# Kernel tuning notes

Measured on AMD Instinct MI355X. Metric: run time of the kernel, lower is better.

The kernel has to match this reference:

```python
import jax, jax.numpy as jnp
import numpy as np

ACT_BIT = 8
W_BIT = 8
EPS = 1e-8


def ste_round(x):
    # straight-through round (matches torch STE quant autograd)
    return x + jax.lax.stop_gradient(jnp.round(x) - x)


def quant_act(x):
    """Per-tensor symmetric 8-bit activation quantization (HAWQ QuantAct)."""
    n = 2 ** (ACT_BIT - 1) - 1  # 127
    x_max = jax.lax.stop_gradient(jnp.max(jnp.abs(x)))
    scale = jnp.maximum(x_max, EPS) / n
    x_int = jnp.clip(ste_round(x / scale), -n - 1, n)
    return x_int * scale, scale


def quant_linear(x_q, act_scale, weight, bias):
    """Per-channel symmetric 8-bit weight quant + integer matmul + fused dequant."""
    n = 2 ** (W_BIT - 1) - 1  # 127
    w_max = jax.lax.stop_gradient(jnp.max(jnp.abs(weight), axis=1, keepdims=True))  # [out,1]
    w_scale = jnp.maximum(w_max, EPS) / n                                            # [out,1]
    w_int = jnp.clip(ste_round(weight / w_scale), -n - 1, n)                         # [out,in]
    bias_scale = w_scale[:, 0] * act_scale                                           # [out]
    b_int = ste_round(bias / bias_scale)                                             # [out]
    x_int = x_q / act_scale                                   # integer-valued float, [..., in]
    out_int = jnp.einsum('...i,oi->...o', x_int, w_int)       # int8-domain GEMM in float
    return (out_int + b_int) * bias_scale                     # fused dequant


def setup_inputs() -> dict:
    key = jax.random.key(0)
    k1, k2, k3 = jax.random.split(key, 3)
    L, B, Q, D, O = 6, 8, 1024, 1024, 1024
    hs = jax.random.normal(k1, (L, B, Q, D), dtype=jnp.float32)
    weight = jax.random.normal(k2, (O, D), dtype=jnp.float32) * 0.02
    bias = jax.random.normal(k3, (O,), dtype=jnp.float32) * 0.02
    return {"hs": hs, "weight": weight, "bias": bias}


def reference(hs, weight, bias):
    x_q, act_scale = quant_act(hs)
    return quant_linear(x_q, act_scale, weight, bias)
```

## Files before the change

### kernel.cpp

```cpp
#include <hip/hip_runtime.h>
#include <stdint.h>

typedef int i32x4 __attribute__((ext_vector_type(4)));

#define K_DIM 1024
#define BM 128
#define BN 128
#define BKK 64
#define NKT (K_DIM / BKK)


__device__ __forceinline__ int quant1(float v, float inv) {
  float t = rintf(v * inv);
  t = fminf(fmaxf(t, -128.0f), 127.0f);
  return (int)t;
}

__device__ __forceinline__ void gld_lds16(const signed char* g, signed char* l) {
  typedef const __attribute__((address_space(1))) unsigned int* gp_t;
  typedef __attribute__((address_space(3))) unsigned int* lp_t;
  __builtin_amdgcn_global_load_lds((gp_t)(const void*)g, (lp_t)(void*)l, 16, 0, 0);
}

#define SB __builtin_amdgcn_sched_barrier(0)
#define BAR __builtin_amdgcn_s_barrier()
#define WAIT_LGKM0 asm volatile("s_waitcnt lgkmcnt(0)" ::: "memory")

__global__ void absmax_part(const float* __restrict__ x, float* __restrict__ parts,
                            long long n4) {
  long long i = (long long)blockIdx.x * blockDim.x + threadIdx.x;
  const long long stride = (long long)gridDim.x * blockDim.x;
  const float4* x4 = (const float4*)x;
  float m = 0.0f;
  for (; i < n4; i += stride) {
    float4 v = x4[i];
    m = fmaxf(m, fmaxf(fmaxf(fabsf(v.x), fabsf(v.y)), fmaxf(fabsf(v.z), fabsf(v.w))));
  }
#pragma unroll
  for (int off = 32; off > 0; off >>= 1) m = fmaxf(m, __shfl_down(m, off, 64));
  __shared__ float sm[4];
  const int lane = threadIdx.x & 63, wid = threadIdx.x >> 6;
  if (lane == 0) sm[wid] = m;
  __syncthreads();
  if (threadIdx.x == 0)
    parts[blockIdx.x] = fmaxf(fmaxf(sm[0], sm[1]), fmaxf(sm[2], sm[3]));
}

__global__ void absmax_fin(const float* __restrict__ parts, unsigned int* __restrict__ amax_u,
                           int nparts) {
  const int t = threadIdx.x;
  float m = 0.0f;
  for (int i = t; i < nparts; i += 256) m = fmaxf(m, parts[i]);
#pragma unroll
  for (int off = 32; off > 0; off >>= 1) m = fmaxf(m, __shfl_down(m, off, 64));
  __shared__ float sm[4];
  const int lane = t & 63, wid = t >> 6;
  if (lane == 0) sm[wid] = m;
  __syncthreads();
  if (t == 0)
    amax_u[0] = __float_as_uint(fmaxf(fmaxf(sm[0], sm[1]), fmaxf(sm[2], sm[3])));
}

__global__ void wquant_kernel(const float* __restrict__ w, const float* __restrict__ bias,
                              const unsigned int* __restrict__ amax_u,
                              signed char* __restrict__ wq,
                              float* __restrict__ bscale, float* __restrict__ bint) {
  const int o = blockIdx.x;
  const int t = threadIdx.x;
  float4 v = ((const float4*)(w + (size_t)o * K_DIM))[t];
  float m = fmaxf(fmaxf(fabsf(v.x), fabsf(v.y)), fmaxf(fabsf(v.z), fabsf(v.w)));
#pragma unroll
  for (int off = 32; off > 0; off >>= 1) m = fmaxf(m, __shfl_down(m, off, 64));
  __shared__ float sm[4];
  __shared__ float s_scale;
  const int lane = t & 63, wid = t >> 6;
  if (lane == 0) sm[wid] = m;
  __syncthreads();
  if (t == 0) {
    float wm = fmaxf(fmaxf(sm[0], sm[1]), fmaxf(sm[2], sm[3]));
    float wsc = fmaxf(wm, 1e-8f) / 127.0f;
    float asc = fmaxf(__uint_as_float(*amax_u), 1e-8f) / 127.0f;
    float bsc = wsc * asc;
    bscale[o] = bsc;
    bint[o] = rintf(bias[o] / bsc);
    s_scale = wsc;
  }
  __syncthreads();
  const float inv = 1.0f / s_scale;
  int q0 = quant1(v.x, inv), q1 = quant1(v.y, inv), q2 = quant1(v.z, inv), q3 = quant1(v.w, inv);
  unsigned int p = (unsigned)(q0 & 255) | ((unsigned)(q1 & 255) << 8) |
                   ((unsigned)(q2 & 255) << 16) | ((unsigned)(q3 & 255) << 24);
  const int F = o >> 4, T = t >> 4;
  const int l = (((t >> 2) & 3) << 4) | (o & 15);
  const int j = (t << 2) & 15;
  *(unsigned int*)(wq + (((size_t)F << 14) + (T << 10) + (l << 4) + j)) = p;
}

__global__ __launch_bounds__(256) void aquant_kernel(
    const float* __restrict__ x, const unsigned int* __restrict__ amax_u,
    uint4* __restrict__ q16) {
  __shared__ unsigned int limg[4096];
  const float asc = fmaxf(__uint_as_float(*amax_u), 1e-8f) / 127.0f;
  const float inv = 1.0f / asc;
  const int F = blockIdx.x;
  const int t = threadIdx.x;
  const int r = t >> 4, kq = t & 15;
  const float* rowp = x + (((size_t)F * 16 + r) << 10);
#pragma unroll
  for (int rep = 0; rep < 16; ++rep) {
    const int fi = rep * 16 + kq;
    float4 v = ((const float4*)rowp)[fi];
    int q0 = quant1(v.x, inv), q1 = quant1(v.y, inv), q2 = quant1(v.z, inv), q3 = quant1(v.w, inv);
    unsigned int p = (unsigned)(q0 & 255) | ((unsigned)(q1 & 255) << 8) |
                     ((unsigned)(q2 & 255) << 16) | ((unsigned)(q3 & 255) << 24);
    const int k0 = fi << 2;
    const int T = k0 >> 6;
    const int l = (((k0 >> 4) & 3) << 4) | r;
    const int j = k0 & 15;
    limg[(T << 8) + (l << 2) + (j >> 2)] = p;
  }
  __syncthreads();
  const uint4* src = (const uint4*)limg;
#pragma unroll
  for (int rep2 = 0; rep2 < 4; ++rep2)
    q16[((size_t)F << 10) + rep2 * 256 + t] = src[rep2 * 256 + t];
}

__global__ __launch_bounds__(256, 3) void gemm_kernel(
    const signed char* __restrict__ A, const signed char* __restrict__ W,
    const float* __restrict__ bscale, const float* __restrict__ bint,
    float* __restrict__ out, int M, int N, int K) {
  extern __shared__ __align__(16) signed char smem[];
  signed char* Abase = smem;

  const int nwg = gridDim.x;
  const int orig = blockIdx.x;
  const int wgid = (orig & 7) * (nwg >> 3) + (orig >> 3);
  const int nbn = N / BN;
  const int bm = wgid / nbn;
  const int bn = wgid % nbn;
  const int m0 = bm * BM, n0 = bn * BN;

  const int tid = threadIdx.x;
  const int lane = tid & 63;
  const int wid = tid >> 6;
  const int wr = wid >> 1;
  const int wc = wid & 1;

  const signed char* gaf = A + (((size_t)(m0 >> 4) + wid) << 14) + (lane << 4);
  const size_t fs4 = (size_t)4 << 14;
  const signed char* gbf = W + (((size_t)(n0 >> 4) + wc * 4) << 14) + (lane << 4);

  i32x4 acc[4][4];
#pragma unroll
  for (int i = 0; i < 4; i++)
#pragma unroll
    for (int j = 0; j < 4; j++) acc[i][j] = (i32x4){0, 0, 0, 0};

  i32x4 af[4];
  i32x4 bfA[4], bfB[4];

#define LOADB(L, tt)                                                           \
  do {                                                                         \
    L[0] = *(const i32x4*)(gbf + ((size_t)0 << 14) + ((tt) << 10));            \
    L[1] = *(const i32x4*)(gbf + ((size_t)1 << 14) + ((tt) << 10));            \
    L[2] = *(const i32x4*)(gbf + ((size_t)2 << 14) + ((tt) << 10));            \
    L[3] = *(const i32x4*)(gbf + ((size_t)3 << 14) + ((tt) << 10));            \
  } while (0)

#define ISSUEA(tt)                                                             \
  do {                                                                         \
    gld_lds16(gaf + ((size_t)(tt) << 10),                                      \
              Abase + ((((tt) & 3) * 8 + wid) << 10));                         \
    gld_lds16(gaf + fs4 + ((size_t)(tt) << 10),                                \
              Abase + ((((tt) & 3) * 8 + wid + 4) << 10));                     \
  } while (0)

#define RD_A(t, i_)                                                            \
  af[i_] = *(const i32x4*)(Abase + ((((t) & 3) * 8 + wr * 4 + (i_)) << 10) + (lane << 4))

#define MFMA16U(U)                                                             \
  do {                                                                         \
    __builtin_amdgcn_s_setprio(1);                                             \
    _Pragma("unroll") for (int i_ = 0; i_ < 4; i_++)                           \
      _Pragma("unroll") for (int j_ = 0; j_ < 4; j_++)                         \
        acc[i_][j_] = __builtin_amdgcn_mfma_i32_16x16x64_i8(                   \
            af[i_], U[j_], acc[i_][j_], 0, 0, 0);                              \
    __builtin_amdgcn_s_setprio(0);                                             \
  } while (0)

#define TILE(t, U, L, DOB, DOA, VMW, DOVM)                                     \
  do {                                                                         \
    if (DOB) LOADB(L, (t) + 1);                                                \
    if (DOA) ISSUEA((t) + 3);                                                  \
    SB;                                                                        \
    RD_A(t, 0); RD_A(t, 1); RD_A(t, 2); RD_A(t, 3);                            \
    MFMA16U(U);                                                                \
    if (DOVM) { asm volatile("s_waitcnt " VMW ::: "memory"); }                 \
    SB; BAR; SB;                                                               \
  } while (0)

  ISSUEA(0); ISSUEA(1); ISSUEA(2);
  LOADB(bfA, 0);
  asm volatile("s_waitcnt vmcnt(8)" ::: "memory");
  SB; BAR; SB;

  TILE(0,  bfA, bfB, 1, 1, "vmcnt(8)", 1);
  TILE(1,  bfB, bfA, 1, 1, "vmcnt(8)", 1);
  TILE(2,  bfA, bfB, 1, 1, "vmcnt(8)", 1);
  TILE(3,  bfB, bfA, 1, 1, "vmcnt(8)", 1);
  TILE(4,  bfA, bfB, 1, 1, "vmcnt(8)", 1);
  TILE(5,  bfB, bfA, 1, 1, "vmcnt(8)", 1);
  TILE(6,  bfA, bfB, 1, 1, "vmcnt(8)", 1);
  TILE(7,  bfB, bfA, 1, 1, "vmcnt(8)", 1);
  TILE(8,  bfA, bfB, 1, 1, "vmcnt(8)", 1);
  TILE(9,  bfB, bfA, 1, 1, "vmcnt(8)", 1);
  TILE(10, bfA, bfB, 1, 1, "vmcnt(8)", 1);
  TILE(11, bfB, bfA, 1, 1, "vmcnt(8)", 1);
  TILE(12, bfA, bfB, 1, 1, "vmcnt(8)", 1);
  TILE(13, bfB, bfA, 1, 0, "vmcnt(6)", 1);
  TILE(14, bfA, bfB, 1, 0, "vmcnt(4)", 1);
  TILE(15, bfB, bfA, 0, 0, "", 0);

#undef TILE
#undef MFMA16U
#undef RD_A
#undef ISSUEA
#undef LOADB

  float* Cst = (float*)smem;
  const int rr = (lane >> 4) * 4;
  const int cc = lane & 15;
#pragma unroll
  for (int h = 0; h < 2; ++h) {
    if (wr == h) {
#pragma unroll
      for (int j = 0; j < 4; j++) {
        const int colL = wc * 64 + j * 16 + cc;
        const float bs = bscale[n0 + colL];
        const float bi = bint[n0 + colL];
#pragma unroll
        for (int i = 0; i < 4; i++)
#pragma unroll
          for (int r = 0; r < 4; r++)
            Cst[(i * 16 + rr + r) * 128 + colL] = ((float)acc[i][j][r] + bi) * bs;
      }
    }
    WAIT_LGKM0;
    BAR;
    const size_t rowbase = (size_t)(m0 + h * 64) * N + n0;
#pragma unroll
    for (int it = 0; it < 8; ++it) {
      const int r_ = it * 8 + wid * 2 + (lane >> 5);
      const int c_ = (lane & 31) * 4;
      float4 v = *(const float4*)&Cst[r_ * 128 + c_];
      *(float4*)&out[rowbase + (size_t)r_ * N + c_] = v;
    }
    WAIT_LGKM0;
    BAR;
  }
}

extern "C" void kernel_launch(void* const* d_in, const int* in_sizes, int n_in,
                              void* d_out, int out_size, void* d_ws, size_t ws_size,
                              hipStream_t stream) {
  const float* hs = (const float*)d_in[0];
  const float* w = (const float*)d_in[1];
  const float* bias = (const float*)d_in[2];
  float* out = (float*)d_out;

  const long long n = (long long)in_sizes[0];
  const int K = K_DIM;
  const int O = in_sizes[2];
  const int M = (int)(n / K);

  char* ws = (char*)d_ws;
  unsigned int* amax_u = (unsigned int*)ws;
  float* parts = (float*)(ws + 1024);
  float* bscale = (float*)(ws + 16384);
  float* bint = (float*)(ws + 20480);
  signed char* wq = (signed char*)(ws + 65536);
  signed char* xq = (signed char*)(ws + 65536 + 1048576);

  const long long n4 = n / 4;
  absmax_part<<<2048, 256, 0, stream>>>(hs, parts, n4);
  absmax_fin<<<1, 256, 0, stream>>>(parts, amax_u, 2048);
  wquant_kernel<<<O, 256, 0, stream>>>(w, bias, amax_u, wq, bscale, bint);
  aquant_kernel<<<M / 16, 256, 0, stream>>>(hs, amax_u, (uint4*)xq);

  const int nblocks = (M / BM) * (O / BN);
  gemm_kernel<<<nblocks, 256, 32768, stream>>>(xq, wq, bscale, bint, out, M, O, K);
}
```

Before: 189.2 us.

## Load A fragments directly from global into registers, dropping LDS staging and barriers

The GEMM main loop no longer stages A tiles in LDS through global_load_lds with a multi-stage ring and per-tile barriers. Each wave now loads its own A and B MFMA fragments straight from global memory into double-buffered registers and alternates load and MFMA sets with no barriers. LDS is kept only as a static buffer for the epilogue transpose. The cost is that each A fragment is fetched by the two waves sharing a row from L2/global instead of once per workgroup, and load latency is hidden only by single-step register prefetch.

```diff
diff --git a/kernel.cpp b/kernel.cpp
--- a/kernel.cpp
+++ b/kernel.cpp
@@ -14,12 +14,6 @@
   float t = rintf(v * inv);
   t = fminf(fmaxf(t, -128.0f), 127.0f);
   return (int)t;
-}
-
-__device__ __forceinline__ void gld_lds16(const signed char* g, signed char* l) {
-  typedef const __attribute__((address_space(1))) unsigned int* gp_t;
-  typedef __attribute__((address_space(3))) unsigned int* lp_t;
-  __builtin_amdgcn_global_load_lds((gp_t)(const void*)g, (lp_t)(void*)l, 16, 0, 0);
 }
 
 #define SB __builtin_amdgcn_sched_barrier(0)
@@ -130,8 +124,7 @@
     const signed char* __restrict__ A, const signed char* __restrict__ W,
     const float* __restrict__ bscale, const float* __restrict__ bint,
     float* __restrict__ out, int M, int N, int K) {
-  extern __shared__ __align__(16) signed char smem[];
-  signed char* Abase = smem;
+  __shared__ __align__(16) float Cst[64 * 128];
 
   const int nwg = gridDim.x;
   const int orig = blockIdx.x;
@@ -147,9 +140,8 @@
   const int wr = wid >> 1;
   const int wc = wid & 1;
 
-  const signed char* gaf = A + (((size_t)(m0 >> 4) + wid) << 14) + (lane << 4);
-  const size_t fs4 = (size_t)4 << 14;
-  const signed char* gbf = W + (((size_t)(n0 >> 4) + wc * 4) << 14) + (lane << 4);
+  const signed char* gA = A + (((size_t)(m0 >> 4) + wr * 4) << 14) + (lane << 4);
+  const signed char* gB = W + (((size_t)(n0 >> 4) + wc * 4) << 14) + (lane << 4);
 
   i32x4 acc[4][4];
 #pragma unroll
@@ -157,82 +149,56 @@
 #pragma unroll
     for (int j = 0; j < 4; j++) acc[i][j] = (i32x4){0, 0, 0, 0};
 
-  i32x4 af[4];
-  i32x4 bfA[4], bfB[4];
-
-#define LOADB(L, tt)                                                           \
+  i32x4 aA[4], aB[4], bA[4], bB[4];
+
+#define LDSET(AR, BR, tt)                                                      \
   do {                                                                         \
-    L[0] = *(const i32x4*)(gbf + ((size_t)0 << 14) + ((tt) << 10));            \
-    L[1] = *(const i32x4*)(gbf + ((size_t)1 << 14) + ((tt) << 10));            \
-    L[2] = *(const i32x4*)(gbf + ((size_t)2 << 14) + ((tt) << 10));            \
-    L[3] = *(const i32x4*)(gbf + ((size_t)3 << 14) + ((tt) << 10));            \
+    AR[0] = *(const i32x4*)(gA + ((size_t)0 << 14) + ((tt) << 10));            \
+    AR[1] = *(const i32x4*)(gA + ((size_t)1 << 14) + ((tt) << 10));            \
+    AR[2] = *(const i32x4*)(gA + ((size_t)2 << 14) + ((tt) << 10));            \
+    AR[3] = *(const i32x4*)(gA + ((size_t)3 << 14) + ((tt) << 10));            \
+    BR[0] = *(const i32x4*)(gB + ((size_t)0 << 14) + ((tt) << 10));            \
+    BR[1] = *(const i32x4*)(gB + ((size_t)1 << 14) + ((tt) << 10));            \
+    BR[2] = *(const i32x4*)(gB + ((size_t)2 << 14) + ((tt) << 10));            \
+    BR[3] = *(const i32x4*)(gB + ((size_t)3 << 14) + ((tt) << 10));            \
   } while (0)
 
-#define ISSUEA(tt)                                                             \
-  do {                                                                         \
-    gld_lds16(gaf + ((size_t)(tt) << 10),                                      \
-              Abase + ((((tt) & 3) * 8 + wid) << 10));                         \
-    gld_lds16(gaf + fs4 + ((size_t)(tt) << 10),                                \
-              Abase + ((((tt) & 3) * 8 + wid + 4) << 10));                     \
-  } while (0)
-
-#define RD_A(t, i_)                                                            \
-  af[i_] = *(const i32x4*)(Abase + ((((t) & 3) * 8 + wr * 4 + (i_)) << 10) + (lane << 4))
-
-#define MFMA16U(U)                                                             \
+#define MFMA16(AR, BR)                                                         \
   do {                                                                         \
     __builtin_amdgcn_s_setprio(1);                                             \
     _Pragma("unroll") for (int i_ = 0; i_ < 4; i_++)                           \
       _Pragma("unroll") for (int j_ = 0; j_ < 4; j_++)                         \
         acc[i_][j_] = __builtin_amdgcn_mfma_i32_16x16x64_i8(                   \
-            af[i_], U[j_], acc[i_][j_], 0, 0, 0);                              \
+            AR[i_], BR[j_], acc[i_][j_], 0, 0, 0);                             \
     __builtin_amdgcn_s_setprio(0);                                             \
   } while (0)
 
-#define TILE(t, U, L, DOB, DOA, VMW, DOVM)                                     \
-  do {                                                                         \
-    if (DOB) LOADB(L, (t) + 1);                                                \
-    if (DOA) ISSUEA((t) + 3);                                                  \
-    SB;                                                                        \
-    RD_A(t, 0); RD_A(t, 1); RD_A(t, 2); RD_A(t, 3);                            \
-    MFMA16U(U);                                                                \
-    if (DOVM) { asm volatile("s_waitcnt " VMW ::: "memory"); }                 \
-    SB; BAR; SB;                                                               \
-  } while (0)
-
-  ISSUEA(0); ISSUEA(1); ISSUEA(2);
-  LOADB(bfA, 0);
-  asm volatile("s_waitcnt vmcnt(8)" ::: "memory");
-  SB; BAR; SB;
-
-  TILE(0,  bfA, bfB, 1, 1, "vmcnt(8)", 1);
-  TILE(1,  bfB, bfA, 1, 1, "vmcnt(8)", 1);
-  TILE(2,  bfA, bfB, 1, 1, "vmcnt(8)", 1);
-  TILE(3,  bfB, bfA, 1, 1, "vmcnt(8)", 1);
-  TILE(4,  bfA, bfB, 1, 1, "vmcnt(8)", 1);
-  TILE(5,  bfB, bfA, 1, 1, "vmcnt(8)", 1);
-  TILE(6,  bfA, bfB, 1, 1, "vmcnt(8)", 1);
-  TILE(7,  bfB, bfA, 1, 1, "vmcnt(8)", 1);
-  TILE(8,  bfA, bfB, 1, 1, "vmcnt(8)", 1);
-  TILE(9,  bfB, bfA, 1, 1, "vmcnt(8)", 1);
-  TILE(10, bfA, bfB, 1, 1, "vmcnt(8)", 1);
-  TILE(11, bfB, bfA, 1, 1, "vmcnt(8)", 1);
-  TILE(12, bfA, bfB, 1, 1, "vmcnt(8)", 1);
-  TILE(13, bfB, bfA, 1, 0, "vmcnt(6)", 1);
-  TILE(14, bfA, bfB, 1, 0, "vmcnt(4)", 1);
-  TILE(15, bfB, bfA, 0, 0, "", 0);
-
-#undef TILE
-#undef MFMA16U
-#undef RD_A
-#undef ISSUEA
-#undef LOADB
-
-  float* Cst = (float*)smem;
+  LDSET(aA, bA, 0);
+  LDSET(aB, bB, 1);  MFMA16(aA, bA);
+  LDSET(aA, bA, 2);  MFMA16(aB, bB);
+  LDSET(aB, bB, 3);  MFMA16(aA, bA);
+  LDSET(aA, bA, 4);  MFMA16(aB, bB);
+  LDSET(aB, bB, 5);  MFMA16(aA, bA);
+  LDSET(aA, bA, 6);  MFMA16(aB, bB);
+  LDSET(aB, bB, 7);  MFMA16(aA, bA);
+  LDSET(aA, bA, 8);  MFMA16(aB, bB);
+  LDSET(aB, bB, 9);  MFMA16(aA, bA);
+  LDSET(aA, bA, 10); MFMA16(aB, bB);
+  LDSET(aB, bB, 11); MFMA16(aA, bA);
+  LDSET(aA, bA, 12); MFMA16(aB, bB);
+  LDSET(aB, bB, 13); MFMA16(aA, bA);
+  LDSET(aA, bA, 14); MFMA16(aB, bB);
+  LDSET(aB, bB, 15); MFMA16(aA, bA);
+  MFMA16(aB, bB);
+
+#undef MFMA16
+#undef LDSET
+
   const int rr = (lane >> 4) * 4;
   const int cc = lane & 15;
 #pragma unroll
   for (int h = 0; h < 2; ++h) {
+    if (h == 1) BAR;
     if (wr == h) {
 #pragma unroll
       for (int j = 0; j < 4; j++) {
@@ -257,7 +223,6 @@
       *(float4*)&out[rowbase + (size_t)r_ * N + c_] = v;
     }
     WAIT_LGKM0;
-    BAR;
   }
 }
 
@@ -289,5 +254,5 @@
   aquant_kernel<<<M / 16, 256, 0, stream>>>(hs, amax_u, (uint4*)xq);
 
   const int nblocks = (M / BM) * (O / BN);
-  gemm_kernel<<<nblocks, 256, 32768, stream>>>(xq, wq, bscale, bint, out, M, O, K);
-}
+  gemm_kernel<<<nblocks, 256, 0, stream>>>(xq, wq, bscale, bint, out, M, O, K);
+}
```

New measurement: 199.4 us. 1.05x slower.

## Enlarge GEMM tiles to 256x256 with 32x32x32 int8 MFMA and direct stores

Applied to the files above, without the earlier changes.

Doubles the GEMM block tile to 256x256 with 512 threads and switches from 16x16x64 to 32x32x32 int8 MFMA. The quantized weight and activation layouts are regrouped into 32-row fragments to match. The epilogue drops the LDS-staged coalesced store and writes scalars straight to global memory. The aim is more operand reuse per loaded byte and fewer, larger MFMAs, at the cost of fewer blocks for the CUs, higher register pressure and less coalesced output writes.

```diff
diff --git a/kernel.cpp b/kernel.cpp
--- a/kernel.cpp
+++ b/kernel.cpp
@@ -2,10 +2,11 @@
 #include <stdint.h>
 
 typedef int i32x4 __attribute__((ext_vector_type(4)));
+typedef int i32x16 __attribute__((ext_vector_type(16)));
 
 #define K_DIM 1024
-#define BM 128
-#define BN 128
+#define BM 256
+#define BN 256
 #define BKK 64
 #define NKT (K_DIM / BKK)
 
@@ -24,7 +25,6 @@
 
 #define SB __builtin_amdgcn_sched_barrier(0)
 #define BAR __builtin_amdgcn_s_barrier()
-#define WAIT_LGKM0 asm volatile("s_waitcnt lgkmcnt(0)" ::: "memory")
 
 __global__ void absmax_part(const float* __restrict__ x, float* __restrict__ parts,
                             long long n4) {
@@ -90,10 +90,10 @@
   int q0 = quant1(v.x, inv), q1 = quant1(v.y, inv), q2 = quant1(v.z, inv), q3 = quant1(v.w, inv);
   unsigned int p = (unsigned)(q0 & 255) | ((unsigned)(q1 & 255) << 8) |
                    ((unsigned)(q2 & 255) << 16) | ((unsigned)(q3 & 255) << 24);
-  const int F = o >> 4, T = t >> 4;
-  const int l = (((t >> 2) & 3) << 4) | (o & 15);
+  const int F = o >> 5, T = t >> 3;
+  const int l = (o & 31) | (((t >> 2) & 1) << 5);
   const int j = (t << 2) & 15;
-  *(unsigned int*)(wq + (((size_t)F << 14) + (T << 10) + (l << 4) + j)) = p;
+  *(unsigned int*)(wq + (((size_t)(F * 32 + T)) << 10) + (l << 4) + j) = p;
 }
 
 __global__ __launch_bounds__(256) void aquant_kernel(
@@ -102,10 +102,11 @@
   __shared__ unsigned int limg[4096];
   const float asc = fmaxf(__uint_as_float(*amax_u), 1e-8f) / 127.0f;
   const float inv = 1.0f / asc;
-  const int F = blockIdx.x;
+  const int b = blockIdx.x;
+  const int F32 = b >> 1, bh = b & 1;
   const int t = threadIdx.x;
   const int r = t >> 4, kq = t & 15;
-  const float* rowp = x + (((size_t)F * 16 + r) << 10);
+  const float* rowp = x + (((size_t)b * 16 + r) << 10);
 #pragma unroll
   for (int rep = 0; rep < 16; ++rep) {
     const int fi = rep * 16 + kq;
@@ -114,19 +115,22 @@
     unsigned int p = (unsigned)(q0 & 255) | ((unsigned)(q1 & 255) << 8) |
                      ((unsigned)(q2 & 255) << 16) | ((unsigned)(q3 & 255) << 24);
     const int k0 = fi << 2;
-    const int T = k0 >> 6;
-    const int l = (((k0 >> 4) & 3) << 4) | r;
+    const int T32 = k0 >> 5;
+    const int hi = (k0 >> 4) & 1;
     const int j = k0 & 15;
-    limg[(T << 8) + (l << 2) + (j >> 2)] = p;
+    limg[(((T32 << 1) | hi) << 6) + (r << 2) + (j >> 2)] = p;
   }
   __syncthreads();
   const uint4* src = (const uint4*)limg;
 #pragma unroll
-  for (int rep2 = 0; rep2 < 4; ++rep2)
-    q16[((size_t)F << 10) + rep2 * 256 + t] = src[rep2 * 256 + t];
-}
-
-__global__ __launch_bounds__(256, 3) void gemm_kernel(
+  for (int rep2 = 0; rep2 < 4; ++rep2) {
+    const int e = rep2 * 256 + t;
+    const int T32 = e >> 5, hs = (e >> 4) & 1, rr = e & 15;
+    q16[(((size_t)(F32 * 32 + T32)) << 6) + (hs * 32 + bh * 16 + rr)] = src[e];
+  }
+}
+
+__global__ __launch_bounds__(512, 2) void gemm_kernel(
     const signed char* __restrict__ A, const signed char* __restrict__ W,
     const float* __restrict__ bscale, const float* __restrict__ bint,
     float* __restrict__ out, int M, int N, int K) {
@@ -144,48 +148,58 @@
   const int tid = threadIdx.x;
   const int lane = tid & 63;
   const int wid = tid >> 6;
-  const int wr = wid >> 1;
-  const int wc = wid & 1;
-
-  const signed char* gaf = A + (((size_t)(m0 >> 4) + wid) << 14) + (lane << 4);
-  const size_t fs4 = (size_t)4 << 14;
-  const signed char* gbf = W + (((size_t)(n0 >> 4) + wc * 4) << 14) + (lane << 4);
-
-  i32x4 acc[4][4];
+  const int wr = wid >> 2;
+  const int wc = wid & 3;
+
+  const signed char* gaf =
+      A + (((size_t)((m0 >> 5) + (wid >> 1)) * 32 + (wid & 1)) << 10) + (lane << 4);
+  const size_t fs8 = (size_t)128 << 10;
+  const signed char* gbf =
+      W + (((size_t)((n0 >> 5) + wc * 2) * 32) << 10) + (lane << 4);
+
+  i32x16 acc[4][2];
 #pragma unroll
   for (int i = 0; i < 4; i++)
 #pragma unroll
-    for (int j = 0; j < 4; j++) acc[i][j] = (i32x4){0, 0, 0, 0};
-
-  i32x4 af[4];
-  i32x4 bfA[4], bfB[4];
+    for (int j = 0; j < 2; j++)
+#pragma unroll
+      for (int r = 0; r < 16; r++) acc[i][j][r] = 0;
+
+  i32x4 af[4][2];
+  i32x4 bA[2][2], bB[2][2];
 
 #define LOADB(L, tt)                                                           \
   do {                                                                         \
-    L[0] = *(const i32x4*)(gbf + ((size_t)0 << 14) + ((tt) << 10));            \
-    L[1] = *(const i32x4*)(gbf + ((size_t)1 << 14) + ((tt) << 10));            \
-    L[2] = *(const i32x4*)(gbf + ((size_t)2 << 14) + ((tt) << 10));            \
-    L[3] = *(const i32x4*)(gbf + ((size_t)3 << 14) + ((tt) << 10));            \
+    L[0][0] = *(const i32x4*)(gbf + (((size_t)(tt) * 2 + 0) << 10));           \
+    L[0][1] = *(const i32x4*)(gbf + (((size_t)(tt) * 2 + 1) << 10));           \
+    L[1][0] = *(const i32x4*)(gbf + ((size_t)1 << 15) + (((size_t)(tt) * 2 + 0) << 10)); \
+    L[1][1] = *(const i32x4*)(gbf + ((size_t)1 << 15) + (((size_t)(tt) * 2 + 1) << 10)); \
   } while (0)
 
 #define ISSUEA(tt)                                                             \
   do {                                                                         \
-    gld_lds16(gaf + ((size_t)(tt) << 10),                                      \
-              Abase + ((((tt) & 3) * 8 + wid) << 10));                         \
-    gld_lds16(gaf + fs4 + ((size_t)(tt) << 10),                                \
-              Abase + ((((tt) & 3) * 8 + wid + 4) << 10));                     \
-  } while (0)
-
-#define RD_A(t, i_)                                                            \
-  af[i_] = *(const i32x4*)(Abase + ((((t) & 3) * 8 + wr * 4 + (i_)) << 10) + (lane << 4))
-
-#define MFMA16U(U)                                                             \
+    gld_lds16(gaf + ((size_t)(tt) << 11),                                      \
+              Abase + ((((tt) & 3) * 16 + wid) << 10));                        \
+    gld_lds16(gaf + fs8 + ((size_t)(tt) << 11),                                \
+              Abase + ((((tt) & 3) * 16 + wid + 8) << 10));                    \
+  } while (0)
+
+#define RD_A(t)                                                                \
+  do {                                                                         \
+    _Pragma("unroll") for (int m_ = 0; m_ < 4; m_++)                           \
+      _Pragma("unroll") for (int k_ = 0; k_ < 2; k_++)                         \
+        af[m_][k_] = *(const i32x4*)(Abase + ((((t) & 3) * 16 +                \
+                        (wr * 4 + m_) * 2 + k_) << 10) + (lane << 4));         \
+  } while (0)
+
+#define MFMA16(U)                                                              \
   do {                                                                         \
     __builtin_amdgcn_s_setprio(1);                                             \
-    _Pragma("unroll") for (int i_ = 0; i_ < 4; i_++)                           \
-      _Pragma("unroll") for (int j_ = 0; j_ < 4; j_++)                         \
-        acc[i_][j_] = __builtin_amdgcn_mfma_i32_16x16x64_i8(                   \
-            af[i_], U[j_], acc[i_][j_], 0, 0, 0);                              \
+    _Pragma("unroll") for (int m_ = 0; m_ < 4; m_++)                           \
+      _Pragma("unroll") for (int g_ = 0; g_ < 2; g_++)                         \
+        _Pragma("unroll") for (int k_ = 0; k_ < 2; k_++)                       \
+          acc[m_][g_] = __builtin_amdgcn_mfma_i32_32x32x32_i8(                 \
+              af[m_][k_], U[g_][k_], acc[m_][g_], 0, 0, 0);                    \
     __builtin_amdgcn_s_setprio(0);                                             \
   } while (0)
 
@@ -194,70 +208,56 @@
     if (DOB) LOADB(L, (t) + 1);                                                \
     if (DOA) ISSUEA((t) + 3);                                                  \
     SB;                                                                        \
-    RD_A(t, 0); RD_A(t, 1); RD_A(t, 2); RD_A(t, 3);                            \
-    MFMA16U(U);                                                                \
+    RD_A(t);                                                                   \
+    MFMA16(U);                                                                 \
     if (DOVM) { asm volatile("s_waitcnt " VMW ::: "memory"); }                 \
     SB; BAR; SB;                                                               \
   } while (0)
 
   ISSUEA(0); ISSUEA(1); ISSUEA(2);
-  LOADB(bfA, 0);
+  LOADB(bA, 0);
   asm volatile("s_waitcnt vmcnt(8)" ::: "memory");
   SB; BAR; SB;
 
-  TILE(0,  bfA, bfB, 1, 1, "vmcnt(8)", 1);
-  TILE(1,  bfB, bfA, 1, 1, "vmcnt(8)", 1);
-  TILE(2,  bfA, bfB, 1, 1, "vmcnt(8)", 1);
-  TILE(3,  bfB, bfA, 1, 1, "vmcnt(8)", 1);
-  TILE(4,  bfA, bfB, 1, 1, "vmcnt(8)", 1);
-  TILE(5,  bfB, bfA, 1, 1, "vmcnt(8)", 1);
-  TILE(6,  bfA, bfB, 1, 1, "vmcnt(8)", 1);
-  TILE(7,  bfB, bfA, 1, 1, "vmcnt(8)", 1);
-  TILE(8,  bfA, bfB, 1, 1, "vmcnt(8)", 1);
-  TILE(9,  bfB, bfA, 1, 1, "vmcnt(8)", 1);
-  TILE(10, bfA, bfB, 1, 1, "vmcnt(8)", 1);
-  TILE(11, bfB, bfA, 1, 1, "vmcnt(8)", 1);
-  TILE(12, bfA, bfB, 1, 1, "vmcnt(8)", 1);
-  TILE(13, bfB, bfA, 1, 0, "vmcnt(6)", 1);
-  TILE(14, bfA, bfB, 1, 0, "vmcnt(4)", 1);
-  TILE(15, bfB, bfA, 0, 0, "", 0);
+  TILE(0,  bA, bB, 1, 1, "vmcnt(8)", 1);
+  TILE(1,  bB, bA, 1, 1, "vmcnt(8)", 1);
+  TILE(2,  bA, bB, 1, 1, "vmcnt(8)", 1);
+  TILE(3,  bB, bA, 1, 1, "vmcnt(8)", 1);
+  TILE(4,  bA, bB, 1, 1, "vmcnt(8)", 1);
+  TILE(5,  bB, bA, 1, 1, "vmcnt(8)", 1);
+  TILE(6,  bA, bB, 1, 1, "vmcnt(8)", 1);
+  TILE(7,  bB, bA, 1, 1, "vmcnt(8)", 1);
+  TILE(8,  bA, bB, 1, 1, "vmcnt(8)", 1);
+  TILE(9,  bB, bA, 1, 1, "vmcnt(8)", 1);
+  TILE(10, bA, bB, 1, 1, "vmcnt(8)", 1);
+  TILE(11, bB, bA, 1, 1, "vmcnt(8)", 1);
+  TILE(12, bA, bB, 1, 1, "vmcnt(8)", 1);
+  TILE(13, bB, bA, 1, 0, "vmcnt(6)", 1);
+  TILE(14, bA, bB, 1, 0, "vmcnt(4)", 1);
+  TILE(15, bB, bA, 0, 0, "", 0);
 
 #undef TILE
-#undef MFMA16U
+#undef MFMA16
 #undef RD_A
 #undef ISSUEA
 #undef LOADB
 
-  float* Cst = (float*)smem;
-  const int rr = (lane >> 4) * 4;
-  const int cc = lane & 15;
-#pragma unroll
-  for (int h = 0; h < 2; ++h) {
-    if (wr == h) {
-#pragma unroll
-      for (int j = 0; j < 4; j++) {
-        const int colL = wc * 64 + j * 16 + cc;
-        const float bs = bscale[n0 + colL];
-        const float bi = bint[n0 + colL];
-#pragma unroll
-        for (int i = 0; i < 4; i++)
-#pragma unroll
-          for (int r = 0; r < 4; r++)
-            Cst[(i * 16 + rr + r) * 128 + colL] = ((float)acc[i][j][r] + bi) * bs;
+  const int cl = lane & 31;
+  const int hi4 = (lane >> 5) << 2;
+#pragma unroll
+  for (int g = 0; g < 2; g++) {
+    const int col = n0 + (wc * 2 + g) * 32 + cl;
+    const float bs = bscale[col];
+    const float bi = bint[col];
+#pragma unroll
+    for (int m = 0; m < 4; m++) {
+      const int rowb = m0 + (wr * 4 + m) * 32 + hi4;
+#pragma unroll
+      for (int r = 0; r < 16; r++) {
+        const int row = rowb + (r & 3) + ((r >> 2) << 3);
+        out[(size_t)row * N + col] = ((float)acc[m][g][r] + bi) * bs;
       }
     }
-    WAIT_LGKM0;
-    BAR;
-    const size_t rowbase = (size_t)(m0 + h * 64) * N + n0;
-#pragma unroll
-    for (int it = 0; it < 8; ++it) {
-      const int r_ = it * 8 + wid * 2 + (lane >> 5);
-      const int c_ = (lane & 31) * 4;
-      float4 v = *(const float4*)&Cst[r_ * 128 + c_];
-      *(float4*)&out[rowbase + (size_t)r_ * N + c_] = v;
-    }
-    WAIT_LGKM0;
-    BAR;
   }
 }
 
@@ -282,6 +282,9 @@
   signed char* wq = (signed char*)(ws + 65536);
   signed char* xq = (signed char*)(ws + 65536 + 1048576);
 
+  hipFuncSetAttribute((const void*)gemm_kernel,
+                      hipFuncAttributeMaxDynamicSharedMemorySize, 65536);
+
   const long long n4 = n / 4;
   absmax_part<<<2048, 256, 0, stream>>>(hs, parts, n4);
   absmax_fin<<<1, 256, 0, stream>>>(parts, amax_u, 2048);
@@ -289,5 +292,5 @@
   aquant_kernel<<<M / 16, 256, 0, stream>>>(hs, amax_u, (uint4*)xq);
 
   const int nblocks = (M / BM) * (O / BN);
-  gemm_kernel<<<nblocks, 256, 32768, stream>>>(xq, wq, bscale, bint, out, M, O, K);
-}
+  gemm_kernel<<<nblocks, 512, 65536, stream>>>(xq, wq, bscale, bint, out, M, O, K);
+}
```

Result: no change. 187.1 us (-1.1%).
